# Performance work log

Hardware: AMD Instinct MI355X
Metric: run time of the kernel (lower is better)

## Reference

```python
import jax, jax.numpy as jnp
import numpy as np

L, B, T, D, H, F = 6, 4, 1024, 512, 8, 2048
DH = D // H
BIAS_DIM = 2
E = 65536
EPS = 1e-3  # LayerNormalization default epsilon in the source


def _ln(x, scale, bias):
    m = jnp.mean(x, axis=-1, keepdims=True)
    v = jnp.mean(jnp.square(x - m), axis=-1, keepdims=True)  # tf.nn.moments: population variance
    return (x - m) * jax.lax.rsqrt(v + EPS) * scale + bias


def setup_inputs() -> dict:
    key = jax.random.key(0)
    ks = jax.random.split(key, 24)
    g = lambda k, shape: (jax.random.normal(k, shape, jnp.float32) * (shape[-1] ** -0.5))
    states = jax.random.normal(ks[0], (B, T, D), jnp.float32)
    # causal mask broadcast over heads: [B, 1, Tq, Tk]
    masks = jnp.tril(jnp.ones((T, T), jnp.float32))[None, None] * jnp.ones((B, 1, 1, 1), jnp.float32)
    # sparse bias edges: columns (edge_type, batch_idx, key_idx, query_idx)
    et = jax.random.randint(ks[1], (E, 1), 0, BIAS_DIM)
    bi = jax.random.randint(ks[2], (E, 1), 0, B)
    ki = jax.random.randint(ks[3], (E, 1), 0, T)
    qi = jax.random.randint(ks[4], (E, 1), 0, T)
    attention_bias = jnp.concatenate([et, bi, ki, qi], axis=1).astype(jnp.int32)
    return dict(
        states=states,
        masks=masks,
        attention_bias=attention_bias,
        Wq=g(ks[5], (L, D, H, DH)),
        Wk=g(ks[6], (L, D, H, DH)),
        Wv=g(ks[7], (L, D, H, DH)),
        Wo=g(ks[8], (L, H, DH, D)),
        Eb=g(ks[9], (L, BIAS_DIM, DH)),
        Es=g(ks[10], (L, DH)),
        ln1_s=jnp.ones((L, D), jnp.float32),
        ln1_b=jnp.zeros((L, D), jnp.float32),
        ln2_s=jnp.ones((L, D), jnp.float32),
        ln2_b=jnp.zeros((L, D), jnp.float32),
        lno_s=jnp.ones((D,), jnp.float32),
        lno_b=jnp.zeros((D,), jnp.float32),
        W1=g(ks[11], (L, D, F)),
        b1=jnp.zeros((L, F), jnp.float32),
        W2=g(ks[12], (L, F, D)),
        b2=jnp.zeros((L, D), jnp.float32),
    )


def reference(states, masks, attention_bias, Wq, Wk, Wv, Wo, Eb, Es,
              ln1_s, ln1_b, ln2_s, ln2_b, lno_s, lno_b, W1, b1, W2, b2):
    FMIN = jnp.finfo(jnp.float32).min
    scale = jnp.float32(DH) ** -0.5
    et, bi, ki, qi = (attention_bias[:, 0], attention_bias[:, 1],
                      attention_bias[:, 2], attention_bias[:, 3])
    for l in range(L):
        # --- self-attention with edge bias ---
        x = _ln(states, ln1_s[l], ln1_b[l])
        q = jnp.einsum('btd,dha->btha', x, Wq[l])
        k = jnp.einsum('btd,dha->btha', x, Wk[l])
        v = jnp.einsum('btd,dha->btha', x, Wv[l])
        alpha = jnp.einsum('bkha,bqha->bhqk', k, q)
        # edge-type embedding -> scalar per edge, scatter into dense [B,q,k] (duplicates sum)
        bias_val = Eb[l][et] @ Es[l]  # [E]
        bias3 = jnp.zeros((B, T, T), jnp.float32).at[bi, ki, qi].add(bias_val)
        alpha = alpha + jnp.einsum('bqk,bkh->bhqk', bias3, k.sum(-1))
        alpha = alpha * scale
        alpha = alpha * masks + (1.0 - jnp.ceil(masks)) * FMIN
        alpha = jax.nn.softmax(alpha, axis=-1) * masks  # mask-softmax-renormalize (no renorm, just re-mask)
        ctx = jnp.einsum('bhqk,bkha->bqha', alpha, v)
        states = states + jnp.einsum('btha,had->btd', ctx, Wo[l])
        # --- FFN ---
        h = jax.nn.relu(_ln(states, ln2_s[l], ln2_b[l]) @ W1[l] + b1[l])
        states = states + h @ W2[l] + b2[l]
    return _ln(states, lno_s, lno_b)
```

## Files before the change

kernel.cpp:

```cpp
#include <hip/hip_runtime.h>
#include <hip/hip_bf16.h>
#include <cstdint>

#define LNUM 6
#define BNUM 4
#define TSEQ 1024
#define DMOD 512
#define HNUM 8
#define FDIM 2048
#define DHEAD 64
#define NEVENTS 65536
#define EPS_LN 1e-3f
#define ATT_SCALE 0.125f

#define GF_ACC 1
#define GF_RELU 2
#define GF_BIAS 4
#define GF_SPLIT 8
#define GF_QKV 16
#define GF_PART 32

typedef float f32x4 __attribute__((ext_vector_type(4)));
typedef short bf16x8 __attribute__((ext_vector_type(8)));
typedef unsigned short u16;
typedef unsigned int u32;

__device__ inline u16 f2bf(float f){
  u32 u = __builtin_bit_cast(u32, f);
  u32 r = (u + 0x7fffu + ((u >> 16) & 1u)) >> 16;
  return (u16)r;
}
__device__ inline float bf2f(u16 u){
  return __builtin_bit_cast(float, (u32)u << 16);
}
__device__ inline void split2(float x, u16 &hi, u16 &lo){
  u16 h = f2bf(x);
  lo = f2bf(x - bf2f(h));
  hi = h;
}
__device__ inline void gload16(const void* g, void* l){
  __builtin_amdgcn_global_load_lds(
      (const __attribute__((address_space(1))) void*)g,
      (__attribute__((address_space(3))) void*)l, 16, 0, 0);
}

__global__ __launch_bounds__(256) void ln_kernel(float* __restrict__ x,
    const float* __restrict__ part, const float* __restrict__ abias,
    const float* __restrict__ s, const float* __restrict__ bsh,
    float* __restrict__ yf, u16* __restrict__ yh, u16* __restrict__ yl, int mode){
  int row = blockIdx.x, tid = threadIdx.x;
  float* xr = x + (size_t)row * DMOD;
  float2 v = *reinterpret_cast<const float2*>(xr + tid*2);
  if (part){
    const size_t MN = (size_t)BNUM*TSEQ*DMOD;
    const size_t o = (size_t)row*DMOD + tid*2;
    float2 p0 = *reinterpret_cast<const float2*>(part + o);
    float2 p1 = *reinterpret_cast<const float2*>(part + MN + o);
    v.x += p0.x + p1.x; v.y += p0.y + p1.y;
    if (abias){
      v.x += abias[tid*2]; v.y += abias[tid*2+1];
    }
    *reinterpret_cast<float2*>(xr + tid*2) = v;
  }
  float sum = v.x + v.y, sq = v.x*v.x + v.y*v.y;
  #pragma unroll
  for (int off = 32; off > 0; off >>= 1){
    sum += __shfl_down(sum, off);
    sq  += __shfl_down(sq, off);
  }
  __shared__ float ss[4], sq2[4];
  int wid = tid >> 6;
  if ((tid & 63) == 0){ ss[wid] = sum; sq2[wid] = sq; }
  __syncthreads();
  sum = ss[0]+ss[1]+ss[2]+ss[3];
  sq  = sq2[0]+sq2[1]+sq2[2]+sq2[3];
  float mean = sum * (1.f/DMOD);
  float var  = sq * (1.f/DMOD) - mean*mean;
  float rstd = rsqrtf(var + EPS_LN);
  float2 sc = *reinterpret_cast<const float2*>(s + tid*2);
  float2 bi = *reinterpret_cast<const float2*>(bsh + tid*2);
  float ox = (v.x - mean)*rstd*sc.x + bi.x;
  float oy = (v.y - mean)*rstd*sc.y + bi.y;
  if (mode == 0){
    u16 h0,l0,h1,l1;
    split2(ox,h0,l0); split2(oy,h1,l1);
    *(u32*)(yh + (size_t)row*DMOD + tid*2) = (u32)h0 | ((u32)h1<<16);
    *(u32*)(yl + (size_t)row*DMOD + tid*2) = (u32)l0 | ((u32)l1<<16);
  } else {
    float2 o; o.x = ox; o.y = oy;
    *reinterpret_cast<float2*>(yf + (size_t)row*DMOD + tid*2) = o;
  }
}

__global__ __launch_bounds__(256) void wsplit5(
    const float* __restrict__ Wq, const float* __restrict__ Wk,
    const float* __restrict__ Wv, const float* __restrict__ Wo,
    const float* __restrict__ W1, int l,
    u16* __restrict__ wqkvh, u16* __restrict__ wqkvl,
    u16* __restrict__ woh,   u16* __restrict__ wol,
    u16* __restrict__ w1h,   u16* __restrict__ w1l){
  __shared__ float T[64][65];
  int id = blockIdx.x;
  const float* src; u16 *dh, *dl; int N, bx, by;
  if (id < 256){
    const int which = id >> 6, sub = id & 63;
    bx = sub & 7; by = sub >> 3; N = 512;
    if (which == 0){ src = Wq; dh = wqkvh;            dl = wqkvl; }
    else if (which == 1){ src = Wk; dh = wqkvh + 512*512; dl = wqkvl + 512*512; }
    else if (which == 2){ src = Wv; dh = wqkvh + 2*512*512; dl = wqkvl + 2*512*512; }
    else { src = Wo; dh = woh; dl = wol; }
    src += (size_t)l*DMOD*DMOD;
  } else {
    id -= 256;
    bx = id & 31; by = id >> 5; N = 2048;
    src = W1 + (size_t)l*DMOD*FDIM; dh = w1h; dl = w1l;
  }
  const int k0 = by*64, n0 = bx*64;
  const int tid = threadIdx.x;
  {
    const int r = tid>>2, cseg = (tid&3)*16;
    const float* sp = src + (size_t)(k0+r)*N + n0 + cseg;
    #pragma unroll
    for (int i = 0; i < 16; i += 4){
      float4 v = *(const float4*)(sp + i);
      T[cseg+i+0][r] = v.x; T[cseg+i+1][r] = v.y;
      T[cseg+i+2][r] = v.z; T[cseg+i+3][r] = v.w;
    }
  }
  __syncthreads();
  const int n = tid>>2, kseg = (tid&3)*16;
  u32 wh[8], wl[8];
  #pragma unroll
  for (int i = 0; i < 8; ++i){
    u16 h0,l0,h1,l1;
    split2(T[n][kseg+2*i], h0, l0);
    split2(T[n][kseg+2*i+1], h1, l1);
    wh[i] = (u32)h0 | ((u32)h1<<16);
    wl[i] = (u32)l0 | ((u32)l1<<16);
  }
  u16* ph = dh + (size_t)(n0+n)*DMOD + k0 + kseg;
  u16* pl = dl + (size_t)(n0+n)*DMOD + k0 + kseg;
  *(uint4*)(ph)   = make_uint4(wh[0],wh[1],wh[2],wh[3]);
  *(uint4*)(ph+8) = make_uint4(wh[4],wh[5],wh[6],wh[7]);
  *(uint4*)(pl)   = make_uint4(wl[0],wl[1],wl[2],wl[3]);
  *(uint4*)(pl+8) = make_uint4(wl[4],wl[5],wl[6],wl[7]);
}

__global__ __launch_bounds__(256) void wsplit(const float* __restrict__ W,
    u16* __restrict__ Thi, u16* __restrict__ Tlo, int K, int N){
  __shared__ float T[64][65];
  const int k0 = blockIdx.y*64, n0 = blockIdx.x*64;
  const int tid = threadIdx.x;
  {
    const int r = tid>>2, cseg = (tid&3)*16;
    const float* src = W + (size_t)(k0+r)*N + n0 + cseg;
    #pragma unroll
    for (int i = 0; i < 16; i += 4){
      float4 v = *(const float4*)(src + i);
      T[cseg+i+0][r] = v.x; T[cseg+i+1][r] = v.y;
      T[cseg+i+2][r] = v.z; T[cseg+i+3][r] = v.w;
    }
  }
  __syncthreads();
  const int n = tid>>2, kseg = (tid&3)*16;
  u32 wh[8], wl[8];
  #pragma unroll
  for (int i = 0; i < 8; ++i){
    u16 h0,l0,h1,l1;
    split2(T[n][kseg+2*i], h0, l0);
    split2(T[n][kseg+2*i+1], h1, l1);
    wh[i] = (u32)h0 | ((u32)h1<<16);
    wl[i] = (u32)l0 | ((u32)l1<<16);
  }
  u16* dh = Thi + (size_t)(n0+n)*K + k0 + kseg;
  u16* dl = Tlo + (size_t)(n0+n)*K + k0 + kseg;
  *(uint4*)(dh)   = make_uint4(wh[0],wh[1],wh[2],wh[3]);
  *(uint4*)(dh+8) = make_uint4(wh[4],wh[5],wh[6],wh[7]);
  *(uint4*)(dl)   = make_uint4(wl[0],wl[1],wl[2],wl[3]);
  *(uint4*)(dl+8) = make_uint4(wl[4],wl[5],wl[6],wl[7]);
}

template<int BN, int NS, int FLAGS>
__global__ __launch_bounds__(256) void gemm_mfma(
    const u16* __restrict__ Ahi, const u16* __restrict__ Alo,
    const u16* __restrict__ Bhi, const u16* __restrict__ Blo,
    const float* __restrict__ bias, float* __restrict__ C,
    u16* __restrict__ Ohi, u16* __restrict__ Olo,
    u16* __restrict__ Vhi, u16* __restrict__ Vlo,
    int M, int N, int K, int kc){
  constexpr int NA  = 16;
  constexpr int NB  = BN/8;
  constexpr int PER = (NA+NB)/4;
  __shared__ __align__(16) unsigned char As[128*128];
  __shared__ __align__(16) unsigned char Bs[BN*128];
  const int tid = threadIdx.x, wid = tid>>6, lane = tid&63;
  const int li = lane&15, g = lane>>4;
  const int nxb = N/BN;
  const int cpx = gridDim.x >> 3;
  const int bid = blockIdx.x;
  const int wg  = (bid&7)*cpx + (bid>>3);
  const int bx = wg % nxb, by = wg / nxb;
  const int m0 = by*128, n0 = bx*BN;
  const int wr = wid>>1, wc = wid&1;
  const int kbeg = blockIdx.y * kc, kend = kbeg + kc;
  f32x4 acc[4][NS] = {};

  for (int k0 = kbeg; k0 < kend; k0 += 32){
    __syncthreads();
    #pragma unroll
    for (int i = 0; i < PER; ++i){
      const int issue = wid*PER + i;
      const bool isA = issue < NA;
      const int ia = isA ? issue : issue - NA;
      const int c = ia*64 + lane;
      const int row = c>>3, slot = c&7;
      const int sg = slot ^ (row&7);
      const u16* base = isA ? (sg < 4 ? Ahi : Alo) : (sg < 4 ? Bhi : Blo);
      const int gr = (isA ? m0 : n0) + row;
      const u16* gp = base + (size_t)gr*K + k0 + (sg&3)*8;
      unsigned char* lp = (isA ? As : Bs) + ia*1024 + lane*16;
      gload16(gp, lp);
    }
    __syncthreads();
    bf16x8 ah[4], al[4], bh[NS], bl[NS];
    #pragma unroll
    for (int ms = 0; ms < 4; ++ms){
      const int r = wr*64 + ms*16 + li; const int x = (r&7)<<4;
      const unsigned char* p = As + r*128;
      ah[ms] = *(const bf16x8*)(p + ((g*16)^x));
      al[ms] = *(const bf16x8*)(p + ((64 + g*16)^x));
    }
    #pragma unroll
    for (int ns = 0; ns < NS; ++ns){
      const int r = wc*(BN/2) + ns*16 + li; const int x = (r&7)<<4;
      const unsigned char* p = Bs + r*128;
      bh[ns] = *(const bf16x8*)(p + ((g*16)^x));
      bl[ns] = *(const bf16x8*)(p + ((64 + g*16)^x));
    }
    #pragma unroll
    for (int ms = 0; ms < 4; ++ms)
      #pragma unroll
      for (int ns = 0; ns < NS; ++ns){
        acc[ms][ns] = __builtin_amdgcn_mfma_f32_16x16x32_bf16(ah[ms], bh[ns], acc[ms][ns], 0, 0, 0);
        acc[ms][ns] = __builtin_amdgcn_mfma_f32_16x16x32_bf16(ah[ms], bl[ns], acc[ms][ns], 0, 0, 0);
        acc[ms][ns] = __builtin_amdgcn_mfma_f32_16x16x32_bf16(al[ms], bh[ns], acc[ms][ns], 0, 0, 0);
      }
  }
  #pragma unroll
  for (int ms = 0; ms < 4; ++ms){
    #pragma unroll
    for (int ns = 0; ns < NS; ++ns){
      #pragma unroll
      for (int r = 0; r < 4; ++r){
        const int m = m0 + wr*64 + ms*16 + g*4 + r;
        const int n = n0 + wc*(BN/2) + ns*16 + li;
        float val = acc[ms][ns][r];
        if (FLAGS & GF_BIAS) val += bias[n];
        if (FLAGS & GF_RELU) val = fmaxf(val, 0.f);
        if (FLAGS & GF_QKV){
          u16 vh, vl; split2(val, vh, vl);
          if (n < 1024){
            const size_t ix = (size_t)m*1024 + n;
            Ohi[ix] = vh; Olo[ix] = vl;
          } else {
            const size_t ix = ((size_t)(m>>10)*DMOD + (n-1024))*TSEQ + (m&1023);
            Vhi[ix] = vh; Vlo[ix] = vl;
          }
        } else if (FLAGS & GF_SPLIT){
          u16 vh, vl; split2(val, vh, vl);
          const size_t ix = (size_t)m*N + n;
          Ohi[ix] = vh; Olo[ix] = vl;
        } else if (FLAGS & GF_PART){
          C[(size_t)blockIdx.y*M*N + (size_t)m*N + n] = val;
        } else {
          const size_t ix = (size_t)m*N + n;
          if (FLAGS & GF_ACC) val += C[ix];
          C[ix] = val;
        }
      }
    }
  }
}

__global__ __launch_bounds__(256) void ksum_kernel(const u16* __restrict__ kh_,
    const u16* __restrict__ kl_, float* __restrict__ ks){
  int idx = blockIdx.x*256 + threadIdx.x;
  const size_t base = (size_t)(idx>>3)*1024 + 512 + (idx&7)*DHEAD;
  const u16* ph = kh_ + base;
  const u16* pl = kl_ + base;
  float s = 0.f;
  #pragma unroll
  for (int a = 0; a < DHEAD; a += 8){
    bf16x8 vh = *(const bf16x8*)(ph + a);
    bf16x8 vl = *(const bf16x8*)(pl + a);
    #pragma unroll
    for (int j = 0; j < 8; ++j) s += bf2f((u16)vh[j]) + bf2f((u16)vl[j]);
  }
  ks[idx] = s;
}

__global__ __launch_bounds__(256) void scatter_kernel(const int* __restrict__ ab,
    const float* __restrict__ Eb, const float* __restrict__ Es, float* __restrict__ bias3){
  __shared__ float d2[2];
  if (threadIdx.x < 2){
    float v = 0.f;
    #pragma unroll
    for (int a = 0; a < DHEAD; ++a) v += Eb[threadIdx.x*DHEAD + a]*Es[a];
    d2[threadIdx.x] = v;
  }
  __syncthreads();
  int e = blockIdx.x*256 + threadIdx.x;
  int4 r = *reinterpret_cast<const int4*>(ab + (size_t)e*4);
  atomicAdd(bias3 + ((size_t)r.y*TSEQ + r.z)*TSEQ + r.w, d2[r.x]);
}

__device__ __forceinline__ void tile_compute(
    const unsigned char* __restrict__ Klh, const unsigned char* __restrict__ Kll,
    const unsigned char* __restrict__ Vh, const unsigned char* __restrict__ Vl,
    unsigned char* __restrict__ Plh, unsigned char* __restrict__ Pll,
    const float* __restrict__ ksl, const float* __restrict__ bb,
    int kt, int rowg0, int wid, int li, int g,
    const bf16x8* qah, const bf16x8* qal,
    f32x4* oacc, float* mrun, float* srun){
  f32x4 sacc[4] = {};
  #pragma unroll
  for (int jb = 0; jb < 4; ++jb){
    const int rb = (jb*16 + li)*128, x = (li & 7) << 4;
    #pragma unroll
    for (int k2 = 0; k2 < 2; ++k2){
      bf16x8 kfh = *(const bf16x8*)(Klh + rb + ((g*16 + k2*64)^x));
      bf16x8 kfl = *(const bf16x8*)(Kll + rb + ((g*16 + k2*64)^x));
      sacc[jb] = __builtin_amdgcn_mfma_f32_16x16x32_bf16(qah[k2], kfh, sacc[jb], 0, 0, 0);
      sacc[jb] = __builtin_amdgcn_mfma_f32_16x16x32_bf16(qah[k2], kfl, sacc[jb], 0, 0, 0);
      sacc[jb] = __builtin_amdgcn_mfma_f32_16x16x32_bf16(qal[k2], kfh, sacc[jb], 0, 0, 0);
    }
  }
  #pragma unroll
  for (int jb = 0; jb < 4; ++jb){
    const int colg = kt + jb*16 + li;
    const float ksv = ksl[jb*16 + li];
    #pragma unroll
    for (int r = 0; r < 4; ++r){
      const int rowg = rowg0 + r;
      float s = (sacc[jb][r] + bb[(size_t)rowg*TSEQ + colg] * ksv) * ATT_SCALE;
      sacc[jb][r] = (colg <= rowg) ? s : -INFINITY;
    }
  }
  #pragma unroll
  for (int r = 0; r < 4; ++r){
    float tm = fmaxf(fmaxf(sacc[0][r], sacc[1][r]), fmaxf(sacc[2][r], sacc[3][r]));
    tm = fmaxf(tm, __shfl_xor(tm, 1));
    tm = fmaxf(tm, __shfl_xor(tm, 2));
    tm = fmaxf(tm, __shfl_xor(tm, 4));
    tm = fmaxf(tm, __shfl_xor(tm, 8));
    const float nm = fmaxf(mrun[r], tm);
    const float fac = __expf(mrun[r] - nm);
    mrun[r] = nm;
    float p0 = __expf(sacc[0][r] - nm);
    float p1 = __expf(sacc[1][r] - nm);
    float p2 = __expf(sacc[2][r] - nm);
    float p3 = __expf(sacc[3][r] - nm);
    float rs = p0 + p1 + p2 + p3;
    rs += __shfl_xor(rs, 1);
    rs += __shfl_xor(rs, 2);
    rs += __shfl_xor(rs, 4);
    rs += __shfl_xor(rs, 8);
    srun[r] = srun[r]*fac + rs;
    oacc[0][r] *= fac; oacc[1][r] *= fac; oacc[2][r] *= fac; oacc[3][r] *= fac;
    const int prow = g*4 + r;
    const int pb = wid*2048 + prow*128, px = (prow & 7) << 4;
    u16 ph0,pl0, ph1,pl1, ph2,pl2, ph3,pl3;
    split2(p0,ph0,pl0); split2(p1,ph1,pl1); split2(p2,ph2,pl2); split2(p3,ph3,pl3);
    *(u16*)(Plh + pb + ((li*2 +  0)^px)) = ph0;
    *(u16*)(Plh + pb + ((li*2 + 32)^px)) = ph1;
    *(u16*)(Plh + pb + ((li*2 + 64)^px)) = ph2;
    *(u16*)(Plh + pb + ((li*2 + 96)^px)) = ph3;
    *(u16*)(Pll + pb + ((li*2 +  0)^px)) = pl0;
    *(u16*)(Pll + pb + ((li*2 + 32)^px)) = pl1;
    *(u16*)(Pll + pb + ((li*2 + 64)^px)) = pl2;
    *(u16*)(Pll + pb + ((li*2 + 96)^px)) = pl3;
  }
  bf16x8 pah[2], pal[2];
  {
    const int pb = wid*2048 + li*128, x = (li & 7) << 4;
    pah[0] = *(const bf16x8*)(Plh + pb + ((g*16     )^x));
    pah[1] = *(const bf16x8*)(Plh + pb + ((g*16 + 64)^x));
    pal[0] = *(const bf16x8*)(Pll + pb + ((g*16     )^x));
    pal[1] = *(const bf16x8*)(Pll + pb + ((g*16 + 64)^x));
  }
  #pragma unroll
  for (int ja = 0; ja < 4; ++ja){
    const int vb = (ja*16 + li)*128, x = (li & 7) << 4;
    #pragma unroll
    for (int k2 = 0; k2 < 2; ++k2){
      bf16x8 vfh = *(const bf16x8*)(Vh + vb + ((g*16 + k2*64)^x));
      bf16x8 vfl = *(const bf16x8*)(Vl + vb + ((g*16 + k2*64)^x));
      oacc[ja] = __builtin_amdgcn_mfma_f32_16x16x32_bf16(pah[k2], vfh, oacc[ja], 0, 0, 0);
      oacc[ja] = __builtin_amdgcn_mfma_f32_16x16x32_bf16(pah[k2], vfl, oacc[ja], 0, 0, 0);
      oacc[ja] = __builtin_amdgcn_mfma_f32_16x16x32_bf16(pal[k2], vfh, oacc[ja], 0, 0, 0);
    }
  }
}

__global__ __launch_bounds__(512, 1) void attn_split(
    const u16* __restrict__ qkh, const u16* __restrict__ qkl,
    const u16* __restrict__ vth, const u16* __restrict__ vtl,
    const float* __restrict__ ksum, const float* __restrict__ bias3,
    u16* __restrict__ ch_, u16* __restrict__ cl_){
  __shared__ __align__(16) unsigned char Klh[8192], Kll[8192], Vh[8192], Vl[8192];
  __shared__ __align__(16) unsigned char Plh[16384], Pll[16384];
  __shared__ float ksl[64];

  const int bid = blockIdx.x;
  const int p = bid & 7, h = (bid >> 3) & 7, b = bid >> 6;
  const int tid = threadIdx.x, wid = tid >> 6, lane = tid & 63;
  const int grp = wid >> 2, wid4 = wid & 3;
  const int li = lane & 15, g = lane >> 4;
  const int q0 = grp ? (15-p)*64 : p*64;
  const int NT = grp ? (16-p) : (p+1);
  const int NB = 16 - p;
  const int row0 = q0 + wid4*16 + g*4;

  bf16x8 qah[2], qal[2];
  {
    const size_t off = (size_t)(b*TSEQ + q0 + wid4*16 + li)*1024 + h*DHEAD;
    #pragma unroll
    for (int k2 = 0; k2 < 2; ++k2){
      qah[k2] = *(const bf16x8*)(qkh + off + g*8 + k2*32);
      qal[k2] = *(const bf16x8*)(qkl + off + g*8 + k2*32);
    }
  }

  f32x4 oacc[4] = {};
  float mrun[4] = {-INFINITY,-INFINITY,-INFINITY,-INFINITY};
  float srun[4] = {0.f,0.f,0.f,0.f};

  const int krow = tid >> 3, part8 = tid & 7;
  const int lbase = krow*128, lx = (krow & 7) << 4;
  const int lslot = (part8*16) ^ lx;
  const float* bb = bias3 + (size_t)b*TSEQ*TSEQ;

  uint4 rkh, rkl, rvh, rvl;
  float ksr = 0.f;
  auto issue = [&](int kt){
    const size_t koff = (size_t)(b*TSEQ + kt + krow)*1024 + 512 + h*DHEAD + part8*8;
    rkh = *(const uint4*)(qkh + koff);
    rkl = *(const uint4*)(qkl + koff);
    const size_t voff = ((size_t)b*DMOD + h*DHEAD + krow)*TSEQ + kt + part8*8;
    rvh = *(const uint4*)(vth + voff);
    rvl = *(const uint4*)(vtl + voff);
    if (tid < 64) ksr = ksum[(size_t)(b*TSEQ + kt + tid)*HNUM + h];
  };

  issue(0);
  for (int it = 0; it < NB; ++it){
    const int kt = it*64;
    *(uint4*)(Klh + lbase + lslot) = rkh;
    *(uint4*)(Kll + lbase + lslot) = rkl;
    *(uint4*)(Vh  + lbase + lslot) = rvh;
    *(uint4*)(Vl  + lbase + lslot) = rvl;
    if (tid < 64) ksl[tid] = ksr;
    __syncthreads();
    if (it + 1 < NB) issue(kt + 64);
    if (it < NT)
      tile_compute(Klh, Kll, Vh, Vl, Plh, Pll, ksl, bb, kt, row0, wid, li, g,
                   qah, qal, oacc, mrun, srun);
    __syncthreads();
  }

  #pragma unroll
  for (int ja = 0; ja < 4; ++ja){
    #pragma unroll
    for (int r = 0; r < 4; ++r){
      const float val = oacc[ja][r] / srun[r];
      u16 vh, vl; split2(val, vh, vl);
      const size_t ix = (size_t)(b*TSEQ + row0 + r)*DMOD + h*DHEAD + ja*16 + li;
      ch_[ix] = vh; cl_[ix] = vl;
    }
  }
}

extern "C" void kernel_launch(void* const* d_in, const int* in_sizes, int n_in,
                              void* d_out, int out_size, void* d_ws, size_t ws_size,
                              hipStream_t stream){
  const float* states0 = (const float*)d_in[0];
  const int*   ab      = (const int*)d_in[2];
  const float* Wq = (const float*)d_in[3];
  const float* Wk = (const float*)d_in[4];
  const float* Wv = (const float*)d_in[5];
  const float* Wo = (const float*)d_in[6];
  const float* Eb = (const float*)d_in[7];
  const float* Es = (const float*)d_in[8];
  const float* ln1_s = (const float*)d_in[9];
  const float* ln1_b = (const float*)d_in[10];
  const float* ln2_s = (const float*)d_in[11];
  const float* ln2_b = (const float*)d_in[12];
  const float* lno_s = (const float*)d_in[13];
  const float* lno_b = (const float*)d_in[14];
  const float* W1 = (const float*)d_in[15];
  const float* b1 = (const float*)d_in[16];
  const float* W2 = (const float*)d_in[17];
  const float* b2 = (const float*)d_in[18];
  float* out = (float*)d_out;

  char* ws = (char*)d_ws;
  const size_t MB = 1024*1024;
  float* states = (float*)(ws);
  u16* xh  = (u16*)(ws + 8*MB);
  u16* xl  = (u16*)(ws + 12*MB);
  u16* qkh = (u16*)(ws + 16*MB);
  u16* qkl = (u16*)(ws + 24*MB);
  u16* vth = (u16*)(ws + 32*MB);
  u16* vtl = (u16*)(ws + 36*MB);
  u16* cth = (u16*)(ws + 40*MB);
  u16* ctl = (u16*)(ws + 44*MB);
  float* ksum  = (float*)(ws + 48*MB);
  float* bias3 = (float*)(ws + 48*MB + 131072);
  char*  wA    = ws + 64*MB + 131072;
  char*  wB    = wA + 4*MB;
  u16* hh = qkh;
  u16* hl = vth;
  float* part = bias3;

  u16* wqkvh = (u16*)(wA);
  u16* wqkvl = (u16*)(wA + 1536*1024);
  u16* woh   = (u16*)(wA + 3*MB);
  u16* wol   = (u16*)(wA + 3*MB + 512*1024);
  u16* w2h   = (u16*)(wA);
  u16* w2l   = (u16*)(wA + 2*MB);
  u16* w1h   = (u16*)(wB);
  u16* w1l   = (u16*)(wB + 2*MB);

  hipMemcpyAsync(states, states0, 8*MB, hipMemcpyDeviceToDevice, stream);

  const int NROW = BNUM*TSEQ;
  dim3 blk(256);
  for (int l = 0; l < LNUM; ++l){
    wsplit5<<<512, blk, 0, stream>>>(Wq, Wk, Wv, Wo, W1, l,
        wqkvh, wqkvl, woh, wol, w1h, w1l);

    ln_kernel<<<NROW, blk, 0, stream>>>(states,
        (l == 0) ? nullptr : part, (l == 0) ? nullptr : b2 + (size_t)(l-1)*DMOD,
        ln1_s + l*DMOD, ln1_b + l*DMOD, nullptr, xh, xl, 0);
    gemm_mfma<128,4, GF_SPLIT|GF_QKV><<<384, blk, 0, stream>>>(
        xh, xl, wqkvh, wqkvl, nullptr, nullptr, qkh, qkl, vth, vtl, NROW, 1536, DMOD, DMOD);
    ksum_kernel<<<(BNUM*TSEQ*HNUM)/256, blk, 0, stream>>>(qkh, qkl, ksum);
    hipMemsetAsync(bias3, 0, (size_t)BNUM*TSEQ*TSEQ*sizeof(float), stream);
    scatter_kernel<<<NEVENTS/256, blk, 0, stream>>>(ab, Eb + (size_t)l*2*DHEAD, Es + (size_t)l*DHEAD, bias3);
    attn_split<<<BNUM*HNUM*8, dim3(512), 0, stream>>>(qkh, qkl, vth, vtl, ksum, bias3, cth, ctl);
    gemm_mfma<64,2, GF_PART><<<dim3(256,2), blk, 0, stream>>>(
        cth, ctl, woh, wol, nullptr, part, nullptr, nullptr, nullptr, nullptr, NROW, DMOD, DMOD, DMOD/2);

    wsplit<<<dim3(8,32), blk, 0, stream>>>(W2 + (size_t)l*FDIM*DMOD, w2h, w2l, FDIM, DMOD);
    ln_kernel<<<NROW, blk, 0, stream>>>(states, part, nullptr,
        ln2_s + l*DMOD, ln2_b + l*DMOD, nullptr, xh, xl, 0);
    gemm_mfma<128,4, GF_BIAS|GF_RELU|GF_SPLIT><<<512, blk, 0, stream>>>(
        xh, xl, w1h, w1l, b1 + (size_t)l*FDIM, nullptr, hh, hl, nullptr, nullptr, NROW, FDIM, DMOD, DMOD);
    gemm_mfma<64,2, GF_PART><<<dim3(256,2), blk, 0, stream>>>(
        hh, hl, w2h, w2l, nullptr, part, nullptr, nullptr, nullptr, nullptr, NROW, DMOD, FDIM, FDIM/2);
  }
  ln_kernel<<<NROW, blk, 0, stream>>>(states, part, b2 + (size_t)(LNUM-1)*DMOD,
      lno_s, lno_b, out, nullptr, nullptr, 1);
}
```

Measured before the change: 1.487 ms.

## Precompute per-type edge counts once and fold W2 split into fused weight kernel

Replaces the per-layer fp32 bias3 memset and atomic scatter with a single pre-loop scatter of per-cell edge-type counts, packed as 8-bit fields in u16 and stored in the output buffer. Attention rebuilds the bias per layer from count and d0/d1 dot products. The W2 weight split moves into the fused weight-split kernel with its own buffer. Attention warps now interleave rows from the two paired query blocks so every warp does equal work and the per-warp tile guard is dropped, but counts above 255 per cell would overflow the 8-bit fields.

```diff
diff --git a/kernel.cpp b/kernel.cpp
--- a/kernel.cpp
+++ b/kernel.cpp
@@ -92,28 +92,33 @@
   }
 }
 
-__global__ __launch_bounds__(256) void wsplit5(
+__global__ __launch_bounds__(256) void wsplit6(
     const float* __restrict__ Wq, const float* __restrict__ Wk,
     const float* __restrict__ Wv, const float* __restrict__ Wo,
-    const float* __restrict__ W1, int l,
+    const float* __restrict__ W1, const float* __restrict__ W2, int l,
     u16* __restrict__ wqkvh, u16* __restrict__ wqkvl,
     u16* __restrict__ woh,   u16* __restrict__ wol,
-    u16* __restrict__ w1h,   u16* __restrict__ w1l){
+    u16* __restrict__ w1h,   u16* __restrict__ w1l,
+    u16* __restrict__ w2h,   u16* __restrict__ w2l){
   __shared__ float T[64][65];
   int id = blockIdx.x;
-  const float* src; u16 *dh, *dl; int N, bx, by;
+  const float* src; u16 *dh, *dl; int N, Kst, bx, by;
   if (id < 256){
     const int which = id >> 6, sub = id & 63;
-    bx = sub & 7; by = sub >> 3; N = 512;
+    bx = sub & 7; by = sub >> 3; N = 512; Kst = 512;
     if (which == 0){ src = Wq; dh = wqkvh;            dl = wqkvl; }
     else if (which == 1){ src = Wk; dh = wqkvh + 512*512; dl = wqkvl + 512*512; }
     else if (which == 2){ src = Wv; dh = wqkvh + 2*512*512; dl = wqkvl + 2*512*512; }
     else { src = Wo; dh = woh; dl = wol; }
     src += (size_t)l*DMOD*DMOD;
+  } else if (id < 512){
+    int sub = id - 256;
+    bx = sub & 31; by = sub >> 5; N = 2048; Kst = 512;
+    src = W1 + (size_t)l*DMOD*FDIM; dh = w1h; dl = w1l;
   } else {
-    id -= 256;
-    bx = id & 31; by = id >> 5; N = 2048;
-    src = W1 + (size_t)l*DMOD*FDIM; dh = w1h; dl = w1l;
+    int sub = id - 512;
+    bx = sub & 7; by = sub >> 3; N = 512; Kst = 2048;
+    src = W2 + (size_t)l*FDIM*DMOD; dh = w2h; dl = w2l;
   }
   const int k0 = by*64, n0 = bx*64;
   const int tid = threadIdx.x;
@@ -138,46 +143,12 @@
     wh[i] = (u32)h0 | ((u32)h1<<16);
     wl[i] = (u32)l0 | ((u32)l1<<16);
   }
-  u16* ph = dh + (size_t)(n0+n)*DMOD + k0 + kseg;
-  u16* pl = dl + (size_t)(n0+n)*DMOD + k0 + kseg;
+  u16* ph = dh + (size_t)(n0+n)*Kst + k0 + kseg;
+  u16* pl = dl + (size_t)(n0+n)*Kst + k0 + kseg;
   *(uint4*)(ph)   = make_uint4(wh[0],wh[1],wh[2],wh[3]);
   *(uint4*)(ph+8) = make_uint4(wh[4],wh[5],wh[6],wh[7]);
   *(uint4*)(pl)   = make_uint4(wl[0],wl[1],wl[2],wl[3]);
   *(uint4*)(pl+8) = make_uint4(wl[4],wl[5],wl[6],wl[7]);
-}
-
-__global__ __launch_bounds__(256) void wsplit(const float* __restrict__ W,
-    u16* __restrict__ Thi, u16* __restrict__ Tlo, int K, int N){
-  __shared__ float T[64][65];
-  const int k0 = blockIdx.y*64, n0 = blockIdx.x*64;
-  const int tid = threadIdx.x;
-  {
-    const int r = tid>>2, cseg = (tid&3)*16;
-    const float* src = W + (size_t)(k0+r)*N + n0 + cseg;
-    #pragma unroll
-    for (int i = 0; i < 16; i += 4){
-      float4 v = *(const float4*)(src + i);
-      T[cseg+i+0][r] = v.x; T[cseg+i+1][r] = v.y;
-      T[cseg+i+2][r] = v.z; T[cseg+i+3][r] = v.w;
-    }
-  }
-  __syncthreads();
-  const int n = tid>>2, kseg = (tid&3)*16;
-  u32 wh[8], wl[8];
-  #pragma unroll
-  for (int i = 0; i < 8; ++i){
-    u16 h0,l0,h1,l1;
-    split2(T[n][kseg+2*i], h0, l0);
-    split2(T[n][kseg+2*i+1], h1, l1);
-    wh[i] = (u32)h0 | ((u32)h1<<16);
-    wl[i] = (u32)l0 | ((u32)l1<<16);
-  }
-  u16* dh = Thi + (size_t)(n0+n)*K + k0 + kseg;
-  u16* dl = Tlo + (size_t)(n0+n)*K + k0 + kseg;
-  *(uint4*)(dh)   = make_uint4(wh[0],wh[1],wh[2],wh[3]);
-  *(uint4*)(dh+8) = make_uint4(wh[4],wh[5],wh[6],wh[7]);
-  *(uint4*)(dl)   = make_uint4(wl[0],wl[1],wl[2],wl[3]);
-  *(uint4*)(dl+8) = make_uint4(wl[4],wl[5],wl[6],wl[7]);
 }
 
 template<int BN, int NS, int FLAGS>
@@ -299,27 +270,22 @@
   ks[idx] = s;
 }
 
-__global__ __launch_bounds__(256) void scatter_kernel(const int* __restrict__ ab,
-    const float* __restrict__ Eb, const float* __restrict__ Es, float* __restrict__ bias3){
-  __shared__ float d2[2];
-  if (threadIdx.x < 2){
-    float v = 0.f;
-    #pragma unroll
-    for (int a = 0; a < DHEAD; ++a) v += Eb[threadIdx.x*DHEAD + a]*Es[a];
-    d2[threadIdx.x] = v;
-  }
-  __syncthreads();
+__global__ __launch_bounds__(256) void scatter_cnt(const int* __restrict__ ab,
+    u32* __restrict__ cntw){
   int e = blockIdx.x*256 + threadIdx.x;
   int4 r = *reinterpret_cast<const int4*>(ab + (size_t)e*4);
-  atomicAdd(bias3 + ((size_t)r.y*TSEQ + r.z)*TSEQ + r.w, d2[r.x]);
+  const size_t cell = ((size_t)r.y*TSEQ + r.z)*TSEQ + r.w;
+  const u32 inc = (r.x ? 0x100u : 1u) << (16*(cell & 1));
+  atomicAdd(cntw + (cell >> 1), inc);
 }
 
 __device__ __forceinline__ void tile_compute(
     const unsigned char* __restrict__ Klh, const unsigned char* __restrict__ Kll,
     const unsigned char* __restrict__ Vh, const unsigned char* __restrict__ Vl,
     unsigned char* __restrict__ Plh, unsigned char* __restrict__ Pll,
-    const float* __restrict__ ksl, const float* __restrict__ bb,
-    int kt, int rowg0, int wid, int li, int g,
+    const float* __restrict__ ksl, const u16* __restrict__ bb,
+    float d0, float e1,
+    int kt, const int* rows4, int wid, int li, int g,
     const bf16x8* qah, const bf16x8* qal,
     f32x4* oacc, float* mrun, float* srun){
   f32x4 sacc[4] = {};
@@ -341,8 +307,10 @@
     const float ksv = ksl[jb*16 + li];
     #pragma unroll
     for (int r = 0; r < 4; ++r){
-      const int rowg = rowg0 + r;
-      float s = (sacc[jb][r] + bb[(size_t)rowg*TSEQ + colg] * ksv) * ATT_SCALE;
+      const int rowg = rows4[r];
+      const u32 c = bb[(size_t)rowg*TSEQ + colg];
+      const float bv = fmaf((float)c, d0, (float)(c >> 8) * e1);
+      float s = (sacc[jb][r] + bv * ksv) * ATT_SCALE;
       sacc[jb][r] = (colg <= rowg) ? s : -INFINITY;
     }
   }
@@ -405,25 +373,40 @@
 __global__ __launch_bounds__(512, 1) void attn_split(
     const u16* __restrict__ qkh, const u16* __restrict__ qkl,
     const u16* __restrict__ vth, const u16* __restrict__ vtl,
-    const float* __restrict__ ksum, const float* __restrict__ bias3,
+    const float* __restrict__ ksum, const u16* __restrict__ cnt,
+    const float* __restrict__ Ebl, const float* __restrict__ Esl,
     u16* __restrict__ ch_, u16* __restrict__ cl_){
   __shared__ __align__(16) unsigned char Klh[8192], Kll[8192], Vh[8192], Vl[8192];
   __shared__ __align__(16) unsigned char Plh[16384], Pll[16384];
   __shared__ float ksl[64];
 
   const int bid = blockIdx.x;
-  const int p = bid & 7, h = (bid >> 3) & 7, b = bid >> 6;
+  const int h = bid & 7, p = (bid >> 3) & 7, b = bid >> 6;
+  const int qA0 = p*64, qB0 = (15-p)*64;
+  const int NB = 16 - p;
   const int tid = threadIdx.x, wid = tid >> 6, lane = tid & 63;
-  const int grp = wid >> 2, wid4 = wid & 3;
   const int li = lane & 15, g = lane >> 4;
-  const int q0 = grp ? (15-p)*64 : p*64;
-  const int NT = grp ? (16-p) : (p+1);
-  const int NB = 16 - p;
-  const int row0 = q0 + wid4*16 + g*4;
+
+  float d0 = 0.f, d1 = 0.f;
+  #pragma unroll 8
+  for (int a = 0; a < DHEAD; ++a){
+    const float e = Esl[a];
+    d0 += Ebl[a] * e;
+    d1 += Ebl[DHEAD + a] * e;
+  }
+  const float e1 = d1 - 256.f*d0;
+
+  const int qrowLi = (li < 8) ? (qA0 + wid*8 + li) : (qB0 + wid*8 + li - 8);
+  int rows4[4];
+  #pragma unroll
+  for (int r = 0; r < 4; ++r){
+    const int i16 = g*4 + r;
+    rows4[r] = (i16 < 8) ? (qA0 + wid*8 + i16) : (qB0 + wid*8 + i16 - 8);
+  }
 
   bf16x8 qah[2], qal[2];
   {
-    const size_t off = (size_t)(b*TSEQ + q0 + wid4*16 + li)*1024 + h*DHEAD;
+    const size_t off = (size_t)(b*TSEQ + qrowLi)*1024 + h*DHEAD;
     #pragma unroll
     for (int k2 = 0; k2 < 2; ++k2){
       qah[k2] = *(const bf16x8*)(qkh + off + g*8 + k2*32);
@@ -436,9 +419,9 @@
   float srun[4] = {0.f,0.f,0.f,0.f};
 
   const int krow = tid >> 3, part8 = tid & 7;
-  const int lbase = krow*128, lx = (krow & 7) << 4;
-  const int lslot = (part8*16) ^ lx;
-  const float* bb = bias3 + (size_t)b*TSEQ*TSEQ;
+  const int lbase = krow*128;
+  const int lslot = ((part8*16) ^ ((krow & 7) << 4));
+  const u16* bb = cnt + (size_t)b*TSEQ*TSEQ;
 
   uint4 rkh, rkl, rvh, rvl;
   float ksr = 0.f;
@@ -462,9 +445,8 @@
     if (tid < 64) ksl[tid] = ksr;
     __syncthreads();
     if (it + 1 < NB) issue(kt + 64);
-    if (it < NT)
-      tile_compute(Klh, Kll, Vh, Vl, Plh, Pll, ksl, bb, kt, row0, wid, li, g,
-                   qah, qal, oacc, mrun, srun);
+    tile_compute(Klh, Kll, Vh, Vl, Plh, Pll, ksl, bb, d0, e1, kt, rows4,
+                 wid, li, g, qah, qal, oacc, mrun, srun);
     __syncthreads();
   }
 
@@ -474,7 +456,7 @@
     for (int r = 0; r < 4; ++r){
       const float val = oacc[ja][r] / srun[r];
       u16 vh, vl; split2(val, vh, vl);
-      const size_t ix = (size_t)(b*TSEQ + row0 + r)*DMOD + h*DHEAD + ja*16 + li;
+      const size_t ix = (size_t)(b*TSEQ + rows4[r])*DMOD + h*DHEAD + ja*16 + li;
       ch_[ix] = vh; cl_[ix] = vl;
     }
   }
@@ -515,29 +497,32 @@
   u16* cth = (u16*)(ws + 40*MB);
   u16* ctl = (u16*)(ws + 44*MB);
   float* ksum  = (float*)(ws + 48*MB);
-  float* bias3 = (float*)(ws + 48*MB + 131072);
+  float* part  = (float*)(ws + 48*MB + 131072);
   char*  wA    = ws + 64*MB + 131072;
   char*  wB    = wA + 4*MB;
+  char*  wC    = wB + 4*MB;
   u16* hh = qkh;
   u16* hl = vth;
-  float* part = bias3;
+  u16* cnt = (u16*)d_out;
 
   u16* wqkvh = (u16*)(wA);
   u16* wqkvl = (u16*)(wA + 1536*1024);
   u16* woh   = (u16*)(wA + 3*MB);
   u16* wol   = (u16*)(wA + 3*MB + 512*1024);
-  u16* w2h   = (u16*)(wA);
-  u16* w2l   = (u16*)(wA + 2*MB);
   u16* w1h   = (u16*)(wB);
   u16* w1l   = (u16*)(wB + 2*MB);
+  u16* w2h   = (u16*)(wC);
+  u16* w2l   = (u16*)(wC + 2*MB);
 
   hipMemcpyAsync(states, states0, 8*MB, hipMemcpyDeviceToDevice, stream);
+  hipMemsetAsync(d_out, 0, (size_t)BNUM*TSEQ*TSEQ*sizeof(u16), stream);
+  scatter_cnt<<<NEVENTS/256, 256, 0, stream>>>(ab, (u32*)d_out);
 
   const int NROW = BNUM*TSEQ;
   dim3 blk(256);
   for (int l = 0; l < LNUM; ++l){
-    wsplit5<<<512, blk, 0, stream>>>(Wq, Wk, Wv, Wo, W1, l,
-        wqkvh, wqkvl, woh, wol, w1h, w1l);
+    wsplit6<<<768, blk, 0, stream>>>(Wq, Wk, Wv, Wo, W1, W2, l,
+        wqkvh, wqkvl, woh, wol, w1h, w1l, w2h, w2l);
 
     ln_kernel<<<NROW, blk, 0, stream>>>(states,
         (l == 0) ? nullptr : part, (l == 0) ? nullptr : b2 + (size_t)(l-1)*DMOD,
@@ -545,13 +530,11 @@
     gemm_mfma<128,4, GF_SPLIT|GF_QKV><<<384, blk, 0, stream>>>(
         xh, xl, wqkvh, wqkvl, nullptr, nullptr, qkh, qkl, vth, vtl, NROW, 1536, DMOD, DMOD);
     ksum_kernel<<<(BNUM*TSEQ*HNUM)/256, blk, 0, stream>>>(qkh, qkl, ksum);
-    hipMemsetAsync(bias3, 0, (size_t)BNUM*TSEQ*TSEQ*sizeof(float), stream);
-    scatter_kernel<<<NEVENTS/256, blk, 0, stream>>>(ab, Eb + (size_t)l*2*DHEAD, Es + (size_t)l*DHEAD, bias3);
-    attn_split<<<BNUM*HNUM*8, dim3(512), 0, stream>>>(qkh, qkl, vth, vtl, ksum, bias3, cth, ctl);
+    attn_split<<<BNUM*HNUM*8, dim3(512), 0, stream>>>(qkh, qkl, vth, vtl, ksum, cnt,
+        Eb + (size_t)l*2*DHEAD, Es + (size_t)l*DHEAD, cth, ctl);
     gemm_mfma<64,2, GF_PART><<<dim3(256,2), blk, 0, stream>>>(
         cth, ctl, woh, wol, nullptr, part, nullptr, nullptr, nullptr, nullptr, NROW, DMOD, DMOD, DMOD/2);
 
-    wsplit<<<dim3(8,32), blk, 0, stream>>>(W2 + (size_t)l*FDIM*DMOD, w2h, w2l, FDIM, DMOD);
     ln_kernel<<<NROW, blk, 0, stream>>>(states, part, nullptr,
         ln2_s + l*DMOD, ln2_b + l*DMOD, nullptr, xh, xl, 0);
     gemm_mfma<128,4, GF_BIAS|GF_RELU|GF_SPLIT><<<512, blk, 0, stream>>>(
```

Result: faster. 1.430 ms (-3.9%).
